# Performance work log

Hardware: AMD Instinct MI355X
Metric: run time of the kernel (lower is better)

The kernel has to match this reference:

```python
import jax, jax.numpy as jnp
import numpy as np

N_NODES = 100000
N_EDGES = 3200000
N_FEAT = 128
DIM = 48
N_CLASS = 18
BN_EPS = 1e-5


def setup_inputs() -> dict:
    key = jax.random.key(0)
    ks = jax.random.split(key, 20)
    x = jax.random.normal(ks[0], (N_NODES, N_FEAT), dtype=jnp.float32)
    edge_index = jax.random.randint(ks[1], (2, N_EDGES), 0, N_NODES, dtype=jnp.int64)

    def lin(k, fan_in, fan_out):
        s = 1.0 / np.sqrt(fan_in)
        kw, kb = jax.random.split(k)
        W = jax.random.uniform(kw, (fan_in, fan_out), jnp.float32, -s, s)
        b = jax.random.uniform(kb, (fan_out,), jnp.float32, -s, s)
        return W, b

    c1_W1, c1_b1 = lin(ks[2], N_FEAT, DIM)
    c1_W2, c1_b2 = lin(ks[3], DIM, DIM)
    c2_W1, c2_b1 = lin(ks[4], DIM, DIM)
    c2_W2, c2_b2 = lin(ks[5], DIM, DIM)
    fc1_W, fc1_b = lin(ks[6], DIM, DIM)
    fc2_W, fc2_b = lin(ks[7], DIM, N_CLASS)

    def bn(k):
        k1, k2, k3, k4 = jax.random.split(k, 4)
        gamma = 1.0 + 0.1 * jax.random.normal(k1, (DIM,), jnp.float32)
        beta = 0.1 * jax.random.normal(k2, (DIM,), jnp.float32)
        mean = 0.1 * jax.random.normal(k3, (DIM,), jnp.float32)
        var = jax.random.uniform(k4, (DIM,), jnp.float32, 0.5, 1.5)
        return gamma, beta, mean, var

    bn1_g, bn1_b, bn1_m, bn1_v = bn(ks[8])
    bn2_g, bn2_b, bn2_m, bn2_v = bn(ks[9])

    return {
        "x": x, "edge_index": edge_index,
        "c1_W1": c1_W1, "c1_b1": c1_b1, "c1_W2": c1_W2, "c1_b2": c1_b2,
        "c2_W1": c2_W1, "c2_b1": c2_b1, "c2_W2": c2_W2, "c2_b2": c2_b2,
        "bn1_g": bn1_g, "bn1_b": bn1_b, "bn1_m": bn1_m, "bn1_v": bn1_v,
        "bn2_g": bn2_g, "bn2_b": bn2_b, "bn2_m": bn2_m, "bn2_v": bn2_v,
        "fc1_W": fc1_W, "fc1_b": fc1_b, "fc2_W": fc2_W, "fc2_b": fc2_b,
    }


def _gine_conv(x, src, dst, W1, b1, W2, b2, eps=0.0):
    # PyG GINEConv (edge_attr absent): message = ReLU(x_j), sum-aggregate to dst,
    # then nn((1+eps)*x + aggr) where nn = Linear-ReLU-Linear.
    msg = jax.nn.relu(x[src])                                  # [E, F]
    aggr = jax.ops.segment_sum(msg, dst, num_segments=x.shape[0])  # [N, F]
    h = (1.0 + eps) * x + aggr
    return jax.nn.relu(h @ W1 + b1) @ W2 + b2


def _bn_eval(x, gamma, beta, mean, var):
    return (x - mean) * (gamma * jax.lax.rsqrt(var + BN_EPS)) + beta


def reference(x, edge_index,
              c1_W1, c1_b1, c1_W2, c1_b2,
              c2_W1, c2_b1, c2_W2, c2_b2,
              bn1_g, bn1_b, bn1_m, bn1_v,
              bn2_g, bn2_b, bn2_m, bn2_v,
              fc1_W, fc1_b, fc2_W, fc2_b):
    src, dst = edge_index[0], edge_index[1]
    h = jax.nn.relu(_gine_conv(x, src, dst, c1_W1, c1_b1, c1_W2, c1_b2))
    h = _bn_eval(h, bn1_g, bn1_b, bn1_m, bn1_v)
    h = jax.nn.relu(_gine_conv(h, src, dst, c2_W1, c2_b1, c2_W2, c2_b2))
    h = _bn_eval(h, bn2_g, bn2_b, bn2_m, bn2_v)
    h = jax.nn.relu(h @ fc1_W + fc1_b)
    # dropout is identity in eval mode
    return h @ fc2_W + fc2_b
```

## Files before the change

kernel.cpp:

```cpp
#include <hip/hip_runtime.h>
#include <hip/hip_fp16.h>

#define N_NODES 100000
#define N_EDGES 3200000
#define N_FEAT  128
#define DIM     48
#define N_CLASS 18
#define BN_EPS  1e-5f

#define PADW 136
#define PADC 72
#define MROW 64

#define BSH    7
#define BROWS  128
#define NBUCK  ((N_NODES + BROWS - 1) / BROWS)
#define BCAP   4608
#define EPB    4096
#define NBLK_E ((N_EDGES + EPB - 1) / EPB)

typedef __attribute__((ext_vector_type(8))) _Float16 f16x8;
typedef __attribute__((ext_vector_type(4))) float f32x4;



__global__ __launch_bounds__(256) void k_bin(const int* __restrict__ ei,
                                             int* __restrict__ bcursor,
                                             unsigned int* __restrict__ pairs) {
    __shared__ int h[NBUCK];
    __shared__ int pos[NBUCK];
    const int t = threadIdx.x;
    const int bs = blockIdx.x * EPB;
    const int ce = min(EPB, N_EDGES - bs);

    int sv[16], dv[16];
    #pragma unroll
    for (int i = 0; i < 16; i++) {
        int e = t + i * 256;
        if (e < ce) { sv[i] = ei[bs + e]; dv[i] = ei[N_EDGES + bs + e]; }
        else { sv[i] = 0; dv[i] = -1; }
    }
    for (int i = t; i < NBUCK; i += 256) h[i] = 0;
    __syncthreads();
    #pragma unroll
    for (int i = 0; i < 16; i++)
        if (dv[i] >= 0) atomicAdd(&h[dv[i] >> BSH], 1);
    __syncthreads();

    for (int b = t; b < NBUCK; b += 256) {
        int cnt = h[b];
        if (cnt > 0) {
            int g = atomicAdd(&bcursor[b], cnt);
            h[b] = b * BCAP + g;
        }
        pos[b] = 0;
    }
    __syncthreads();

    #pragma unroll
    for (int i = 0; i < 16; i++) {
        if (dv[i] >= 0) {
            int b = dv[i] >> BSH;
            int p = atomicAdd(&pos[b], 1);
            pairs[h[b] + p] = ((unsigned int)sv[i] << 7) | (unsigned int)(dv[i] & (BROWS - 1));
        }
    }
}


__global__ __launch_bounds__(256) void k_sort(const unsigned int* __restrict__ pairs,
                                              const int* __restrict__ bcursor,
                                              int* __restrict__ row_beg,
                                              int* __restrict__ row_end,
                                              int* __restrict__ sorted_src) {
    __shared__ int histw[4 * BROWS];
    __shared__ int woff[4 * BROWS];
    __shared__ int tot[BROWS];
    __shared__ int scn[BROWS];
    __shared__ int beg[BROWS];
    const int t = threadIdx.x;
    const int wid = t >> 6;
    const int b = blockIdx.x;
    const int nbase = b << BSH;
    const int start_w = b * BCAP;
    const int cnt = bcursor[b];

    for (int i = t; i < 4 * BROWS; i += 256) histw[i] = 0;
    __syncthreads();
    for (int e = start_w + t; e < start_w + cnt; e += 256)
        atomicAdd(&histw[wid * BROWS + (pairs[e] & (BROWS - 1))], 1);
    __syncthreads();

    if (t < BROWS) {
        int run = 0;
        #pragma unroll
        for (int w = 0; w < 4; w++) {
            woff[w * BROWS + t] = run;
            run += histw[w * BROWS + t];
        }
        tot[t] = run;
        scn[t] = run;
    }
    __syncthreads();
    for (int off = 1; off < BROWS; off <<= 1) {
        int v = 0;
        if (t < BROWS && t >= off) v = scn[t - off];
        __syncthreads();
        if (t < BROWS) scn[t] += v;
        __syncthreads();
    }
    if (t < BROWS) {
        int rb = start_w + scn[t] - tot[t];
        beg[t] = rb;
        int n = nbase + t;
        if (n < N_NODES) {
            row_beg[n] = rb;
            row_end[n] = rb + tot[t];
        }
    }
    __syncthreads();
    if (t < BROWS) {
        #pragma unroll
        for (int w = 0; w < 4; w++)
            histw[w * BROWS + t] = beg[t] + woff[w * BROWS + t];
    }
    __syncthreads();
    for (int e = start_w + t; e < start_w + cnt; e += 256) {
        unsigned int p = pairs[e];
        int node = p & (BROWS - 1);
        int idx = atomicAdd(&histw[wid * BROWS + node], 1);
        sorted_src[idx] = (int)(p >> 7);
    }
}


__global__ __launch_bounds__(256) void k_g1(const float* __restrict__ x,
                                            const float* __restrict__ W1,
                                            float* __restrict__ t1,
                                            __half* __restrict__ t2) {
    __shared__ _Float16 sX[64 * PADW];
    __shared__ _Float16 sW[DIM * PADW];
    const int t = threadIdx.x;
    const int base = blockIdx.x * 64;
    const int wid = t >> 6, lane = t & 63;

    for (int idx = t; idx < DIM * (N_FEAT / 2); idx += 256) {
        int c = idx >> 6;
        int kk = (idx & 63) * 2;
        *(__half2*)&sW[c * PADW + kk] =
            __floats2half2_rn(W1[kk * DIM + c], W1[(kk + 1) * DIM + c]);
    }
    #pragma unroll
    for (int i = 0; i < 8; i++) {
        int idx = t + i * 256;
        int row = idx >> 5, kq = idx & 31;
        float4 v = make_float4(0.f, 0.f, 0.f, 0.f);
        if (base + row < N_NODES) v = ((const float4*)x)[(base + row) * 32 + kq];
        *(__half2*)&sX[row * PADW + kq * 4]     = __floats2half2_rn(v.x, v.y);
        *(__half2*)&sX[row * PADW + kq * 4 + 2] = __floats2half2_rn(v.z, v.w);
    }
    __syncthreads();

    const int r16 = wid * 16;
    const int lrow = lane & 15;
    const int lk = (lane >> 4) * 8;

    f32x4 acc1[3], acc2[3];
    #pragma unroll
    for (int c = 0; c < 3; c++) {
        acc1[c] = (f32x4){0.f, 0.f, 0.f, 0.f};
        acc2[c] = (f32x4){0.f, 0.f, 0.f, 0.f};
    }

    #pragma unroll
    for (int ks = 0; ks < 4; ks++) {
        f16x8 a = *(const f16x8*)&sX[(r16 + lrow) * PADW + ks * 32 + lk];
        f16x8 ra;
        #pragma unroll
        for (int j = 0; j < 8; j++)
            ra[j] = a[j] > (_Float16)0 ? a[j] : (_Float16)0;
        #pragma unroll
        for (int c = 0; c < 3; c++) {
            f16x8 b = *(const f16x8*)&sW[(c * 16 + lrow) * PADW + ks * 32 + lk];
            acc1[c] = __builtin_amdgcn_mfma_f32_16x16x32_f16(a,  b, acc1[c], 0, 0, 0);
            acc2[c] = __builtin_amdgcn_mfma_f32_16x16x32_f16(ra, b, acc2[c], 0, 0, 0);
        }
    }

    const int orow = r16 + (lane >> 4) * 4;
    const int ocol = lane & 15;
    #pragma unroll
    for (int q = 0; q < 4; q++) {
        int gr = base + orow + q;
        if (gr < N_NODES) {
            #pragma unroll
            for (int c = 0; c < 3; c++) {
                t1[gr * DIM + c * 16 + ocol] = acc1[c][q];
                t2[gr * MROW + c * 16 + ocol] = __float2half(acc2[c][q]);
            }
        }
    }
}


__device__ inline float2 h2tof2(unsigned int u) {
    __half2 h = *reinterpret_cast<__half2*>(&u);
    return __half22float2(h);
}

__global__ __launch_bounds__(256) void k_aggr(const float* tlin,
                                              const uint2* __restrict__ tmsg8,
                                              const int* __restrict__ row_beg,
                                              const int* __restrict__ row_end,
                                              const int* __restrict__ ssrc,
                                              const float* __restrict__ bias,
                                              float* out) {
    const int t = threadIdx.x;
    const int wid = t >> 6, lane = t & 63;
    const int sub = lane / 12;
    const int fl  = lane - sub * 12;
    int n = blockIdx.x * 20 + wid * 5 + sub;
    const bool act = (sub < 5) && (n < N_NODES);
    int start = 0, end = 0;
    if (act) { start = row_beg[n]; end = row_end[n]; }

    float ax = 0.f, ay = 0.f, az = 0.f, aw = 0.f;
    int e = start;
    for (; e + 8 <= end; e += 8) {
        int s0 = ssrc[e], s1 = ssrc[e + 1], s2 = ssrc[e + 2], s3 = ssrc[e + 3];
        int s4 = ssrc[e + 4], s5 = ssrc[e + 5], s6 = ssrc[e + 6], s7 = ssrc[e + 7];
        uint2 v0 = tmsg8[s0 * 16 + fl];
        uint2 v1 = tmsg8[s1 * 16 + fl];
        uint2 v2 = tmsg8[s2 * 16 + fl];
        uint2 v3 = tmsg8[s3 * 16 + fl];
        uint2 v4 = tmsg8[s4 * 16 + fl];
        uint2 v5 = tmsg8[s5 * 16 + fl];
        uint2 v6 = tmsg8[s6 * 16 + fl];
        uint2 v7 = tmsg8[s7 * 16 + fl];
        float2 f;
        f = h2tof2(v0.x); ax += f.x; ay += f.y;  f = h2tof2(v0.y); az += f.x; aw += f.y;
        f = h2tof2(v1.x); ax += f.x; ay += f.y;  f = h2tof2(v1.y); az += f.x; aw += f.y;
        f = h2tof2(v2.x); ax += f.x; ay += f.y;  f = h2tof2(v2.y); az += f.x; aw += f.y;
        f = h2tof2(v3.x); ax += f.x; ay += f.y;  f = h2tof2(v3.y); az += f.x; aw += f.y;
        f = h2tof2(v4.x); ax += f.x; ay += f.y;  f = h2tof2(v4.y); az += f.x; aw += f.y;
        f = h2tof2(v5.x); ax += f.x; ay += f.y;  f = h2tof2(v5.y); az += f.x; aw += f.y;
        f = h2tof2(v6.x); ax += f.x; ay += f.y;  f = h2tof2(v6.y); az += f.x; aw += f.y;
        f = h2tof2(v7.x); ax += f.x; ay += f.y;  f = h2tof2(v7.y); az += f.x; aw += f.y;
    }
    for (; e < end; e++) {
        int s = ssrc[e];
        uint2 v = tmsg8[s * 16 + fl];
        float2 f;
        f = h2tof2(v.x); ax += f.x; ay += f.y;
        f = h2tof2(v.y); az += f.x; aw += f.y;
    }
    if (act) {
        float4 base = ((const float4*)tlin)[n * 12 + fl];
        float4 bi   = ((const float4*)bias)[fl];
        float4 r;
        r.x = fmaxf(base.x + ax + bi.x, 0.f);
        r.y = fmaxf(base.y + ay + bi.y, 0.f);
        r.z = fmaxf(base.z + az + bi.z, 0.f);
        r.w = fmaxf(base.w + aw + bi.w, 0.f);
        ((float4*)out)[n * 12 + fl] = r;
    }
}


__global__ __launch_bounds__(256) void k_chain1(const float* u,
                                                const float* __restrict__ W2,
                                                const float* __restrict__ b2,
                                                const float* __restrict__ bng,
                                                const float* __restrict__ bnb,
                                                const float* __restrict__ bnm,
                                                const float* __restrict__ bnv,
                                                const float* __restrict__ W1n,
                                                float* t3,
                                                __half* __restrict__ t4) {
    __shared__ _Float16 sU[64 * PADC];
    __shared__ _Float16 sG[64 * PADC];
    __shared__ _Float16 sW2t[DIM * PADC];
    __shared__ _Float16 sW1t[DIM * PADC];
    __shared__ float sb2[DIM], ssc[DIM], ssh[DIM];
    const int t = threadIdx.x;
    const int base = blockIdx.x * 64;
    const int wid = t >> 6, lane = t & 63;

    if (t < DIM) {
        sb2[t] = b2[t];
        float sc = bng[t] * rsqrtf(bnv[t] + BN_EPS);
        ssc[t] = sc;
        ssh[t] = bnb[t] - bnm[t] * sc;
    }
    for (int idx = t; idx < DIM * 24; idx += 256) {
        int c = idx / 24, kk = (idx - c * 24) * 2;
        sW2t[c * PADC + kk]     = (_Float16)W2[kk * DIM + c];
        sW2t[c * PADC + kk + 1] = (_Float16)W2[(kk + 1) * DIM + c];
        sW1t[c * PADC + kk]     = (_Float16)W1n[kk * DIM + c];
        sW1t[c * PADC + kk + 1] = (_Float16)W1n[(kk + 1) * DIM + c];
    }
    for (int idx = t; idx < DIM * 16; idx += 256) {
        int c = idx >> 4, j = idx & 15;
        sW2t[c * PADC + 48 + j] = (_Float16)0;
        sW1t[c * PADC + 48 + j] = (_Float16)0;
    }
    for (int idx = t; idx < 64 * 16; idx += 256) {
        int r = idx >> 4, j = idx & 15;
        sU[r * PADC + 48 + j] = (_Float16)0;
        sG[r * PADC + 48 + j] = (_Float16)0;
    }
    for (int idx = t; idx < 64 * 24; idx += 256) {
        int row = idx / 24, kk = (idx - row * 24) * 2;
        float2 v = make_float2(0.f, 0.f);
        if (base + row < N_NODES) v = *(const float2*)&u[(base + row) * DIM + kk];
        sU[row * PADC + kk]     = (_Float16)v.x;
        sU[row * PADC + kk + 1] = (_Float16)v.y;
    }
    __syncthreads();

    const int r16 = wid * 16;
    const int lrow = lane & 15;
    const int lk = (lane >> 4) * 8;
    const int orow = r16 + (lane >> 4) * 4;
    const int ocol = lane & 15;

    f32x4 av[3];
    #pragma unroll
    for (int c = 0; c < 3; c++) av[c] = (f32x4){0.f, 0.f, 0.f, 0.f};
    #pragma unroll
    for (int ks = 0; ks < 2; ks++) {
        f16x8 a = *(const f16x8*)&sU[(r16 + lrow) * PADC + ks * 32 + lk];
        #pragma unroll
        for (int c = 0; c < 3; c++) {
            f16x8 b = *(const f16x8*)&sW2t[(c * 16 + lrow) * PADC + ks * 32 + lk];
            av[c] = __builtin_amdgcn_mfma_f32_16x16x32_f16(a, b, av[c], 0, 0, 0);
        }
    }
    #pragma unroll
    for (int c = 0; c < 3; c++) {
        int col = c * 16 + ocol;
        float bb = sb2[col], sc = ssc[col], sh = ssh[col];
        #pragma unroll
        for (int q = 0; q < 4; q++) {
            float rl = fmaxf(av[c][q] + bb, 0.f);
            sG[(orow + q) * PADC + col] = (_Float16)(rl * sc + sh);
        }
    }
    __syncthreads();

    f32x4 a3[3], a4[3];
    #pragma unroll
    for (int c = 0; c < 3; c++) {
        a3[c] = (f32x4){0.f, 0.f, 0.f, 0.f};
        a4[c] = (f32x4){0.f, 0.f, 0.f, 0.f};
    }
    #pragma unroll
    for (int ks = 0; ks < 2; ks++) {
        f16x8 a = *(const f16x8*)&sG[(r16 + lrow) * PADC + ks * 32 + lk];
        f16x8 ra;
        #pragma unroll
        for (int j = 0; j < 8; j++)
            ra[j] = a[j] > (_Float16)0 ? a[j] : (_Float16)0;
        #pragma unroll
        for (int c = 0; c < 3; c++) {
            f16x8 b = *(const f16x8*)&sW1t[(c * 16 + lrow) * PADC + ks * 32 + lk];
            a3[c] = __builtin_amdgcn_mfma_f32_16x16x32_f16(a,  b, a3[c], 0, 0, 0);
            a4[c] = __builtin_amdgcn_mfma_f32_16x16x32_f16(ra, b, a4[c], 0, 0, 0);
        }
    }
    #pragma unroll
    for (int q = 0; q < 4; q++) {
        int gr = base + orow + q;
        if (gr < N_NODES) {
            #pragma unroll
            for (int c = 0; c < 3; c++) {
                t3[gr * DIM + c * 16 + ocol] = a3[c][q];
                t4[gr * MROW + c * 16 + ocol] = __float2half(a4[c][q]);
            }
        }
    }
}


__global__ __launch_bounds__(256) void k_chain2(const float* __restrict__ u2,
                                                const float* __restrict__ W2,
                                                const float* __restrict__ b2,
                                                const float* __restrict__ bng,
                                                const float* __restrict__ bnb,
                                                const float* __restrict__ bnm,
                                                const float* __restrict__ bnv,
                                                const float* __restrict__ fc1W,
                                                const float* __restrict__ fc1b,
                                                const float* __restrict__ fc2W,
                                                const float* __restrict__ fc2b,
                                                float* __restrict__ out) {
    __shared__ _Float16 sA[64 * PADC];
    __shared__ _Float16 sG[64 * PADC];
    __shared__ _Float16 sWa[DIM * PADC];
    __shared__ _Float16 sWb[DIM * PADC];
    __shared__ _Float16 sWc[32 * PADC];
    __shared__ float sb2[DIM], ssc[DIM], ssh[DIM], sfb1[DIM], sfb2[N_CLASS];
    const int t = threadIdx.x;
    const int base = blockIdx.x * 64;
    const int wid = t >> 6, lane = t & 63;

    if (t < DIM) {
        sb2[t] = b2[t];
        float sc = bng[t] * rsqrtf(bnv[t] + BN_EPS);
        ssc[t] = sc;
        ssh[t] = bnb[t] - bnm[t] * sc;
        sfb1[t] = fc1b[t];
    }
    if (t >= 64 && t < 64 + N_CLASS) sfb2[t - 64] = fc2b[t - 64];

    for (int idx = t; idx < DIM * 24; idx += 256) {
        int c = idx / 24, kk = (idx - c * 24) * 2;
        sWa[c * PADC + kk]     = (_Float16)W2[kk * DIM + c];
        sWa[c * PADC + kk + 1] = (_Float16)W2[(kk + 1) * DIM + c];
        sWb[c * PADC + kk]     = (_Float16)fc1W[kk * DIM + c];
        sWb[c * PADC + kk + 1] = (_Float16)fc1W[(kk + 1) * DIM + c];
    }
    for (int idx = t; idx < DIM * 16; idx += 256) {
        int c = idx >> 4, j = idx & 15;
        sWa[c * PADC + 48 + j] = (_Float16)0;
        sWb[c * PADC + 48 + j] = (_Float16)0;
    }
    for (int idx = t; idx < N_CLASS * DIM; idx += 256) {
        int c = idx / DIM, k = idx - c * DIM;
        sWc[c * PADC + k] = (_Float16)fc2W[k * N_CLASS + c];
    }
    for (int idx = t; idx < 32 * 16; idx += 256) {
        int c = idx >> 4, j = idx & 15;
        sWc[c * PADC + 48 + j] = (_Float16)0;
    }
    for (int idx = t; idx < 14 * 48; idx += 256) {
        int c = 18 + idx / 48, k = idx - (idx / 48) * 48;
        sWc[c * PADC + k] = (_Float16)0;
    }
    for (int idx = t; idx < 64 * 16; idx += 256) {
        int r = idx >> 4, j = idx & 15;
        sA[r * PADC + 48 + j] = (_Float16)0;
        sG[r * PADC + 48 + j] = (_Float16)0;
    }
    for (int idx = t; idx < 64 * 24; idx += 256) {
        int row = idx / 24, kk = (idx - row * 24) * 2;
        float2 v = make_float2(0.f, 0.f);
        if (base + row < N_NODES) v = *(const float2*)&u2[(base + row) * DIM + kk];
        sA[row * PADC + kk]     = (_Float16)v.x;
        sA[row * PADC + kk + 1] = (_Float16)v.y;
    }
    __syncthreads();

    const int r16 = wid * 16;
    const int lrow = lane & 15;
    const int lk = (lane >> 4) * 8;
    const int orow = r16 + (lane >> 4) * 4;
    const int ocol = lane & 15;

    {
        f32x4 av[3];
        #pragma unroll
        for (int c = 0; c < 3; c++) av[c] = (f32x4){0.f, 0.f, 0.f, 0.f};
        #pragma unroll
        for (int ks = 0; ks < 2; ks++) {
            f16x8 a = *(const f16x8*)&sA[(r16 + lrow) * PADC + ks * 32 + lk];
            #pragma unroll
            for (int c = 0; c < 3; c++) {
                f16x8 b = *(const f16x8*)&sWa[(c * 16 + lrow) * PADC + ks * 32 + lk];
                av[c] = __builtin_amdgcn_mfma_f32_16x16x32_f16(a, b, av[c], 0, 0, 0);
            }
        }
        #pragma unroll
        for (int c = 0; c < 3; c++) {
            int col = c * 16 + ocol;
            float bb = sb2[col], sc = ssc[col], sh = ssh[col];
            #pragma unroll
            for (int q = 0; q < 4; q++) {
                float rl = fmaxf(av[c][q] + bb, 0.f);
                sG[(orow + q) * PADC + col] = (_Float16)(rl * sc + sh);
            }
        }
    }
    __syncthreads();

    {
        f32x4 az[3];
        #pragma unroll
        for (int c = 0; c < 3; c++) az[c] = (f32x4){0.f, 0.f, 0.f, 0.f};
        #pragma unroll
        for (int ks = 0; ks < 2; ks++) {
            f16x8 a = *(const f16x8*)&sG[(r16 + lrow) * PADC + ks * 32 + lk];
            #pragma unroll
            for (int c = 0; c < 3; c++) {
                f16x8 b = *(const f16x8*)&sWb[(c * 16 + lrow) * PADC + ks * 32 + lk];
                az[c] = __builtin_amdgcn_mfma_f32_16x16x32_f16(a, b, az[c], 0, 0, 0);
            }
        }
        __syncthreads();
        #pragma unroll
        for (int c = 0; c < 3; c++) {
            int col = c * 16 + ocol;
            float bb = sfb1[col];
            #pragma unroll
            for (int q = 0; q < 4; q++)
                sA[(orow + q) * PADC + col] = (_Float16)fmaxf(az[c][q] + bb, 0.f);
        }
    }
    __syncthreads();

    {
        f32x4 ao[2];
        #pragma unroll
        for (int c = 0; c < 2; c++) ao[c] = (f32x4){0.f, 0.f, 0.f, 0.f};
        #pragma unroll
        for (int ks = 0; ks < 2; ks++) {
            f16x8 a = *(const f16x8*)&sA[(r16 + lrow) * PADC + ks * 32 + lk];
            #pragma unroll
            for (int c = 0; c < 2; c++) {
                f16x8 b = *(const f16x8*)&sWc[(c * 16 + lrow) * PADC + ks * 32 + lk];
                ao[c] = __builtin_amdgcn_mfma_f32_16x16x32_f16(a, b, ao[c], 0, 0, 0);
            }
        }
        #pragma unroll
        for (int q = 0; q < 4; q++) {
            int gr = base + orow + q;
            if (gr < N_NODES) {
                #pragma unroll
                for (int c = 0; c < 2; c++) {
                    int col = c * 16 + ocol;
                    if (col < N_CLASS)
                        out[gr * N_CLASS + col] = ao[c][q] + sfb2[col];
                }
            }
        }
    }
}


extern "C" void kernel_launch(void* const* d_in, const int* in_sizes, int n_in,
                              void* d_out, int out_size, void* d_ws, size_t ws_size,
                              hipStream_t stream) {
    const float* x     = (const float*)d_in[0];
    const int*   ei    = (const int*)d_in[1];
    const float* c1_W1 = (const float*)d_in[2];
    const float* c1_b1 = (const float*)d_in[3];
    const float* c1_W2 = (const float*)d_in[4];
    const float* c1_b2 = (const float*)d_in[5];
    const float* c2_W1 = (const float*)d_in[6];
    const float* c2_b1 = (const float*)d_in[7];
    const float* c2_W2 = (const float*)d_in[8];
    const float* c2_b2 = (const float*)d_in[9];
    const float* bn1_g = (const float*)d_in[10];
    const float* bn1_b = (const float*)d_in[11];
    const float* bn1_m = (const float*)d_in[12];
    const float* bn1_v = (const float*)d_in[13];
    const float* bn2_g = (const float*)d_in[14];
    const float* bn2_b = (const float*)d_in[15];
    const float* bn2_m = (const float*)d_in[16];
    const float* bn2_v = (const float*)d_in[17];
    const float* fc1_W = (const float*)d_in[18];
    const float* fc1_b = (const float*)d_in[19];
    const float* fc2_W = (const float*)d_in[20];
    const float* fc2_b = (const float*)d_in[21];
    float* out = (float*)d_out;

    char* ws = (char*)d_ws;
    size_t o = 0;
    auto take = [&](size_t bytes) {
        void* p = ws + o;
        o = (o + bytes + 255) & ~(size_t)255;
        return p;
    };
    unsigned int* pairs = (unsigned int*)take((size_t)NBUCK * BCAP * 4);
    int*  sorted_src    = (int*)take((size_t)NBUCK * BCAP * 4);
    int*  row_beg       = (int*)take((size_t)N_NODES * 4);
    int*  row_end       = (int*)take((size_t)N_NODES * 4);
    int*  bcursor       = (int*)take((size_t)NBUCK * 4);
    float*  t1          = (float*)take((size_t)N_NODES * DIM * 4);
    __half* t2h         = (__half*)take((size_t)N_NODES * MROW * 2);
    (void)ws_size; (void)in_sizes; (void)n_in; (void)out_size;

    const int NB64 = (N_NODES + 63) / 64;
    const int NB20 = (N_NODES + 19) / 20;

    hipMemsetAsync(bcursor, 0, (size_t)NBUCK * 4, stream);
    k_bin<<<NBLK_E, 256, 0, stream>>>(ei, bcursor, pairs);
    k_sort<<<NBUCK, 256, 0, stream>>>(pairs, bcursor, row_beg, row_end, sorted_src);

    k_g1<<<NB64, 256, 0, stream>>>(x, c1_W1, t1, t2h);
    k_aggr<<<NB20, 256, 0, stream>>>(t1, (const uint2*)t2h, row_beg, row_end, sorted_src, c1_b1, t1);
    k_chain1<<<NB64, 256, 0, stream>>>(t1, c1_W2, c1_b2, bn1_g, bn1_b, bn1_m, bn1_v,
                                       c2_W1, t1, t2h);
    k_aggr<<<NB20, 256, 0, stream>>>(t1, (const uint2*)t2h, row_beg, row_end, sorted_src, c2_b1, t1);
    k_chain2<<<NB64, 256, 0, stream>>>(t1, c2_W2, c2_b2, bn2_g, bn2_b, bn2_m, bn2_v,
                                       fc1_W, fc1_b, fc2_W, fc2_b, out);
}
```

Measured before the change: 272.1 us.

## Fuse neighbor aggregation into the per-layer MLP chain kernels

The separate aggregation kernels are removed. Each chain kernel now gathers neighbor messages for its own 64-row tile, adds bias and ReLU, and writes the result as fp16 straight into shared memory for the MFMA stage. This drops two launches and the fp32 round trip of the aggregated features through global memory. A second fp16 message buffer is added so the gather does not read data the same kernel is overwriting. The trade-off is that the latency-bound gather now runs inside blocks that hold a lot of shared memory, which may lower occupancy. The 5-nodes-per-wave mapping also leaves lanes idle on the last iteration.

```diff
diff --git a/kernel.cpp b/kernel.cpp
--- a/kernel.cpp
+++ b/kernel.cpp
@@ -208,25 +208,12 @@
     return __half22float2(h);
 }
 
-__global__ __launch_bounds__(256) void k_aggr(const float* tlin,
-                                              const uint2* __restrict__ tmsg8,
-                                              const int* __restrict__ row_beg,
-                                              const int* __restrict__ row_end,
-                                              const int* __restrict__ ssrc,
-                                              const float* __restrict__ bias,
-                                              float* out) {
-    const int t = threadIdx.x;
-    const int wid = t >> 6, lane = t & 63;
-    const int sub = lane / 12;
-    const int fl  = lane - sub * 12;
-    int n = blockIdx.x * 20 + wid * 5 + sub;
-    const bool act = (sub < 5) && (n < N_NODES);
-    int start = 0, end = 0;
-    if (act) { start = row_beg[n]; end = row_end[n]; }
-
-    float ax = 0.f, ay = 0.f, az = 0.f, aw = 0.f;
-    int e = start;
-    for (; e + 8 <= end; e += 8) {
+__device__ __forceinline__ void gather48(const uint2* __restrict__ tmsg8,
+                                         const int* __restrict__ ssrc,
+                                         int st, int en, int fl,
+                                         float& ax, float& ay, float& az, float& aw) {
+    int e = st;
+    for (; e + 8 <= en; e += 8) {
         int s0 = ssrc[e], s1 = ssrc[e + 1], s2 = ssrc[e + 2], s3 = ssrc[e + 3];
         int s4 = ssrc[e + 4], s5 = ssrc[e + 5], s6 = ssrc[e + 6], s7 = ssrc[e + 7];
         uint2 v0 = tmsg8[s0 * 16 + fl];
@@ -247,36 +234,31 @@
         f = h2tof2(v6.x); ax += f.x; ay += f.y;  f = h2tof2(v6.y); az += f.x; aw += f.y;
         f = h2tof2(v7.x); ax += f.x; ay += f.y;  f = h2tof2(v7.y); az += f.x; aw += f.y;
     }
-    for (; e < end; e++) {
+    for (; e < en; e++) {
         int s = ssrc[e];
         uint2 v = tmsg8[s * 16 + fl];
         float2 f;
         f = h2tof2(v.x); ax += f.x; ay += f.y;
         f = h2tof2(v.y); az += f.x; aw += f.y;
     }
-    if (act) {
-        float4 base = ((const float4*)tlin)[n * 12 + fl];
-        float4 bi   = ((const float4*)bias)[fl];
-        float4 r;
-        r.x = fmaxf(base.x + ax + bi.x, 0.f);
-        r.y = fmaxf(base.y + ay + bi.y, 0.f);
-        r.z = fmaxf(base.z + az + bi.z, 0.f);
-        r.w = fmaxf(base.w + aw + bi.w, 0.f);
-        ((float4*)out)[n * 12 + fl] = r;
-    }
-}
-
-
-__global__ __launch_bounds__(256) void k_chain1(const float* u,
-                                                const float* __restrict__ W2,
-                                                const float* __restrict__ b2,
-                                                const float* __restrict__ bng,
-                                                const float* __restrict__ bnb,
-                                                const float* __restrict__ bnm,
-                                                const float* __restrict__ bnv,
-                                                const float* __restrict__ W1n,
-                                                float* t3,
-                                                __half* __restrict__ t4) {
+}
+
+
+__global__ __launch_bounds__(256) void k_chain1f(const float* tlin,
+                                                 const uint2* __restrict__ tmsg8,
+                                                 const int* __restrict__ row_beg,
+                                                 const int* __restrict__ row_end,
+                                                 const int* __restrict__ ssrc,
+                                                 const float* __restrict__ ab,
+                                                 const float* __restrict__ W2,
+                                                 const float* __restrict__ b2,
+                                                 const float* __restrict__ bng,
+                                                 const float* __restrict__ bnb,
+                                                 const float* __restrict__ bnm,
+                                                 const float* __restrict__ bnv,
+                                                 const float* __restrict__ W1n,
+                                                 float* t3,
+                                                 __half* __restrict__ t4) {
     __shared__ _Float16 sU[64 * PADC];
     __shared__ _Float16 sG[64 * PADC];
     __shared__ _Float16 sW2t[DIM * PADC];
@@ -285,6 +267,7 @@
     const int t = threadIdx.x;
     const int base = blockIdx.x * 64;
     const int wid = t >> 6, lane = t & 63;
+    const int sub = lane / 12, fl = lane - sub * 12;
 
     if (t < DIM) {
         sb2[t] = b2[t];
@@ -309,12 +292,29 @@
         sU[r * PADC + 48 + j] = (_Float16)0;
         sG[r * PADC + 48 + j] = (_Float16)0;
     }
-    for (int idx = t; idx < 64 * 24; idx += 256) {
-        int row = idx / 24, kk = (idx - row * 24) * 2;
-        float2 v = make_float2(0.f, 0.f);
-        if (base + row < N_NODES) v = *(const float2*)&u[(base + row) * DIM + kk];
-        sU[row * PADC + kk]     = (_Float16)v.x;
-        sU[row * PADC + kk + 1] = (_Float16)v.y;
+
+    for (int it = 0; it < 4; it++) {
+        int r = it * 5 + sub;
+        bool actn = (sub < 5) && (r < 16);
+        int n_loc = wid * 16 + r;
+        int n = base + n_loc;
+        float ax = 0.f, ay = 0.f, az = 0.f, aw = 0.f;
+        int st = 0, en = 0;
+        if (actn && n < N_NODES) { st = row_beg[n]; en = row_end[n]; }
+        gather48(tmsg8, ssrc, st, en, fl, ax, ay, az, aw);
+        if (actn) {
+            float4 r4 = make_float4(0.f, 0.f, 0.f, 0.f);
+            if (n < N_NODES) {
+                float4 bse = ((const float4*)tlin)[n * 12 + fl];
+                float4 bi  = ((const float4*)ab)[fl];
+                r4.x = fmaxf(bse.x + ax + bi.x, 0.f);
+                r4.y = fmaxf(bse.y + ay + bi.y, 0.f);
+                r4.z = fmaxf(bse.z + az + bi.z, 0.f);
+                r4.w = fmaxf(bse.w + aw + bi.w, 0.f);
+            }
+            *(__half2*)&sU[n_loc * PADC + fl * 4]     = __floats2half2_rn(r4.x, r4.y);
+            *(__half2*)&sU[n_loc * PADC + fl * 4 + 2] = __floats2half2_rn(r4.z, r4.w);
+        }
     }
     __syncthreads();
 
@@ -382,18 +382,23 @@
 }
 
 
-__global__ __launch_bounds__(256) void k_chain2(const float* __restrict__ u2,
-                                                const float* __restrict__ W2,
-                                                const float* __restrict__ b2,
-                                                const float* __restrict__ bng,
-                                                const float* __restrict__ bnb,
-                                                const float* __restrict__ bnm,
-                                                const float* __restrict__ bnv,
-                                                const float* __restrict__ fc1W,
-                                                const float* __restrict__ fc1b,
-                                                const float* __restrict__ fc2W,
-                                                const float* __restrict__ fc2b,
-                                                float* __restrict__ out) {
+__global__ __launch_bounds__(256) void k_chain2f(const float* __restrict__ tlin,
+                                                 const uint2* __restrict__ tmsg8,
+                                                 const int* __restrict__ row_beg,
+                                                 const int* __restrict__ row_end,
+                                                 const int* __restrict__ ssrc,
+                                                 const float* __restrict__ ab,
+                                                 const float* __restrict__ W2,
+                                                 const float* __restrict__ b2,
+                                                 const float* __restrict__ bng,
+                                                 const float* __restrict__ bnb,
+                                                 const float* __restrict__ bnm,
+                                                 const float* __restrict__ bnv,
+                                                 const float* __restrict__ fc1W,
+                                                 const float* __restrict__ fc1b,
+                                                 const float* __restrict__ fc2W,
+                                                 const float* __restrict__ fc2b,
+                                                 float* __restrict__ out) {
     __shared__ _Float16 sA[64 * PADC];
     __shared__ _Float16 sG[64 * PADC];
     __shared__ _Float16 sWa[DIM * PADC];
@@ -403,6 +408,7 @@
     const int t = threadIdx.x;
     const int base = blockIdx.x * 64;
     const int wid = t >> 6, lane = t & 63;
+    const int sub = lane / 12, fl = lane - sub * 12;
 
     if (t < DIM) {
         sb2[t] = b2[t];
@@ -442,12 +448,29 @@
         sA[r * PADC + 48 + j] = (_Float16)0;
         sG[r * PADC + 48 + j] = (_Float16)0;
     }
-    for (int idx = t; idx < 64 * 24; idx += 256) {
-        int row = idx / 24, kk = (idx - row * 24) * 2;
-        float2 v = make_float2(0.f, 0.f);
-        if (base + row < N_NODES) v = *(const float2*)&u2[(base + row) * DIM + kk];
-        sA[row * PADC + kk]     = (_Float16)v.x;
-        sA[row * PADC + kk + 1] = (_Float16)v.y;
+
+    for (int it = 0; it < 4; it++) {
+        int r = it * 5 + sub;
+        bool actn = (sub < 5) && (r < 16);
+        int n_loc = wid * 16 + r;
+        int n = base + n_loc;
+        float ax = 0.f, ay = 0.f, az = 0.f, aw = 0.f;
+        int st = 0, en = 0;
+        if (actn && n < N_NODES) { st = row_beg[n]; en = row_end[n]; }
+        gather48(tmsg8, ssrc, st, en, fl, ax, ay, az, aw);
+        if (actn) {
+            float4 r4 = make_float4(0.f, 0.f, 0.f, 0.f);
+            if (n < N_NODES) {
+                float4 bse = ((const float4*)tlin)[n * 12 + fl];
+                float4 bi  = ((const float4*)ab)[fl];
+                r4.x = fmaxf(bse.x + ax + bi.x, 0.f);
+                r4.y = fmaxf(bse.y + ay + bi.y, 0.f);
+                r4.z = fmaxf(bse.z + az + bi.z, 0.f);
+                r4.w = fmaxf(bse.w + aw + bi.w, 0.f);
+            }
+            *(__half2*)&sA[n_loc * PADC + fl * 4]     = __floats2half2_rn(r4.x, r4.y);
+            *(__half2*)&sA[n_loc * PADC + fl * 4 + 2] = __floats2half2_rn(r4.z, r4.w);
+        }
     }
     __syncthreads();
 
@@ -578,20 +601,20 @@
     int*  bcursor       = (int*)take((size_t)NBUCK * 4);
     float*  t1          = (float*)take((size_t)N_NODES * DIM * 4);
     __half* t2h         = (__half*)take((size_t)N_NODES * MROW * 2);
+    __half* t4h         = (__half*)take((size_t)N_NODES * MROW * 2);
     (void)ws_size; (void)in_sizes; (void)n_in; (void)out_size;
 
     const int NB64 = (N_NODES + 63) / 64;
-    const int NB20 = (N_NODES + 19) / 20;
 
     hipMemsetAsync(bcursor, 0, (size_t)NBUCK * 4, stream);
     k_bin<<<NBLK_E, 256, 0, stream>>>(ei, bcursor, pairs);
     k_sort<<<NBUCK, 256, 0, stream>>>(pairs, bcursor, row_beg, row_end, sorted_src);
 
     k_g1<<<NB64, 256, 0, stream>>>(x, c1_W1, t1, t2h);
-    k_aggr<<<NB20, 256, 0, stream>>>(t1, (const uint2*)t2h, row_beg, row_end, sorted_src, c1_b1, t1);
-    k_chain1<<<NB64, 256, 0, stream>>>(t1, c1_W2, c1_b2, bn1_g, bn1_b, bn1_m, bn1_v,
-                                       c2_W1, t1, t2h);
-    k_aggr<<<NB20, 256, 0, stream>>>(t1, (const uint2*)t2h, row_beg, row_end, sorted_src, c2_b1, t1);
-    k_chain2<<<NB64, 256, 0, stream>>>(t1, c2_W2, c2_b2, bn2_g, bn2_b, bn2_m, bn2_v,
-                                       fc1_W, fc1_b, fc2_W, fc2_b, out);
-}
+    k_chain1f<<<NB64, 256, 0, stream>>>(t1, (const uint2*)t2h, row_beg, row_end, sorted_src,
+                                        c1_b1, c1_W2, c1_b2, bn1_g, bn1_b, bn1_m, bn1_v,
+                                        c2_W1, t1, t4h);
+    k_chain2f<<<NB64, 256, 0, stream>>>(t1, (const uint2*)t4h, row_beg, row_end, sorted_src,
+                                        c2_b1, c2_W2, c2_b2, bn2_g, bn2_b, bn2_m, bn2_v,
+                                        fc1_W, fc1_b, fc2_W, fc2_b, out);
+}
```

Measured after the change: 303.1 us. 1.11x slower.
